# Performance work log

Measured on AMD Instinct MI355X. Metric: run time of the kernel, lower is better.

## Reference

```python
import jax, jax.numpy as jnp
import numpy as np

D_MODEL = 512
NUM_HEADS = 8
HEAD_DIM = D_MODEL // NUM_HEADS  # 64
EMBEDDING_DIM = 512  # undefined global EmbeddingDim in source -> d_model
EVENT_DIM = 388      # undefined global EventDim in source -> MIDI event vocab
B, T = 2, 2048


def setup_inputs() -> dict:
    key = jax.random.key(0)
    ks = jax.random.split(key, 12)
    sc = 0.02
    v = jax.random.normal(ks[0], (B, T, D_MODEL), jnp.float32)
    k = jax.random.normal(ks[1], (B, T, D_MODEL), jnp.float32)
    q = jax.random.normal(ks[2], (B, T, D_MODEL), jnp.float32)
    mask = jnp.tril(jnp.ones((T, T), jnp.float32))  # causal mask, broadcasts to [H,B,T,T]
    Wq = jax.random.normal(ks[3], (D_MODEL, HEAD_DIM), jnp.float32) * sc
    bq = jnp.zeros((HEAD_DIM,), jnp.float32)
    Wk = jax.random.normal(ks[4], (D_MODEL, HEAD_DIM), jnp.float32) * sc
    bk = jnp.zeros((HEAD_DIM,), jnp.float32)
    Wv = jax.random.normal(ks[5], (D_MODEL, HEAD_DIM), jnp.float32) * sc
    bv = jnp.zeros((HEAD_DIM,), jnp.float32)
    E = jax.random.normal(ks[6], (NUM_HEADS, T, HEAD_DIM), jnp.float32) * sc
    Wo = jax.random.normal(ks[7], (D_MODEL, EMBEDDING_DIM), jnp.float32) * sc
    bo = jnp.zeros((EMBEDDING_DIM,), jnp.float32)
    Wl = jax.random.normal(ks[8], (EMBEDDING_DIM, EVENT_DIM), jnp.float32) * sc
    bl = jnp.zeros((EVENT_DIM,), jnp.float32)
    return {"v": v, "k": k, "q": q, "mask": mask, "Wq": Wq, "bq": bq,
            "Wk": Wk, "bk": bk, "Wv": Wv, "bv": bv, "E": E,
            "Wo": Wo, "bo": bo, "Wl": Wl, "bl": bl}


def _skew(S):
    # S: [H,B,T,T] -> Music-Transformer skew via left-pad, reshape, slice
    H, Bb, Tt, _ = S.shape
    S = jnp.pad(S, ((0, 0), (0, 0), (0, 0), (1, 0)))          # [H,B,T,T+1]
    S = S.reshape(H, Bb, Tt + 1, Tt)                           # [H,B,T+1,T]
    return S[:, :, 1:]                                         # [H,B,T,T]


def reference(v, k, q, mask, Wq, bq, Wk, bk, Wv, bv, E, Wo, bo, Wl, bl):
    # The source applies the SAME Dense per head, so all heads share q/k/v projections
    qh = q @ Wq + bq  # [B,T,hd]
    kh = k @ Wk + bk  # [B,T,hd]
    vh = v @ Wv + bv  # [B,T,hd]
    # relative-position scores per head: Q @ E^T then skew
    S = jnp.einsum('btd,hsd->hbts', qh, E)  # [H,B,T,T]
    S = _skew(S)
    qk = jnp.einsum('btd,bsd->bts', qh, kh)  # [B,T,T], identical across heads
    attn = (qk[None] + S) / np.sqrt(HEAD_DIM)  # [H,B,T,T]
    attn = attn * mask - jnp.asarray(1e10, attn.dtype) * (1.0 - mask)
    score = jax.nn.softmax(attn, axis=-1)
    ctx = jnp.einsum('hbts,bsd->hbtd', score, vh)  # [H,B,T,hd]
    ctx = jnp.transpose(ctx, (1, 2, 0, 3)).reshape(ctx.shape[1], ctx.shape[2], -1)  # [B,T,d_model]
    ctx = jax.nn.relu(ctx @ Wo + bo)  # [B,T,EmbeddingDim]
    logits = ctx @ Wl + bl            # [B,T,EventDim]
    return logits
```

## Files before the change

kernel.cpp:

```cpp
#include <hip/hip_runtime.h>
#include <hip/hip_bf16.h>


#define B_ 2
#define T_ 2048
#define DM_ 512
#define H_ 8
#define HD_ 64
#define ED_ 512
#define EV_ 388
#define BT_ (B_ * T_)

typedef __attribute__((ext_vector_type(8))) short short8;
typedef __attribute__((ext_vector_type(4))) float floatx4;

#define MFMA(a, b, c) __builtin_amdgcn_mfma_f32_16x16x32_bf16((a), (b), (c), 0, 0, 0)

__device__ __forceinline__ float bfs(unsigned short s) {
  union { unsigned int i; float f; } v; v.i = ((unsigned int)s) << 16; return v.f;
}
__device__ __forceinline__ unsigned short f2bf(float f) {
  __hip_bfloat16 h = __float2bfloat16(f);
  union { __hip_bfloat16 h; unsigned short u; } v; v.h = h; return v.u;
}
__device__ __forceinline__ float ldf(const void* p, int i, bool isbf) {
  return isbf ? bfs(((const unsigned short*)p)[i]) : ((const float*)p)[i];
}
__device__ __forceinline__ bool det_bf(const unsigned int* mask) {
  return mask[0] != 0x3F800000u;
}
__device__ __forceinline__ void gl_lds16(const unsigned short* g, void* l) {
  __builtin_amdgcn_global_load_lds(
      (const __attribute__((address_space(1))) void*)g,
      (__attribute__((address_space(3))) void*)l, 16, 0, 0);
}

__global__ __launch_bounds__(256) void prep_kernel(
    const void* __restrict__ E, const void* __restrict__ Wq,
    const void* __restrict__ Wk, const void* __restrict__ Wv,
    const void* __restrict__ Wo, const void* __restrict__ Wl,
    const unsigned int* __restrict__ mask,
    unsigned short* __restrict__ E_c, unsigned short* __restrict__ WqT,
    unsigned short* __restrict__ WkT, unsigned short* __restrict__ WvT,
    unsigned short* __restrict__ WoT, unsigned short* __restrict__ WlT) {
  const bool isbf = det_bf(mask);
  const int tid = threadIdx.x;
  int bi = blockIdx.x;
  if (bi < 1024) {
    const int i0 = (bi * 256 + tid) * 4;
    if (isbf) {
      *(uint2*)&E_c[i0] = *(const uint2*)((const unsigned short*)E + i0);
    } else {
      float4 f = *(const float4*)((const float*)E + i0);
      unsigned short p[4] = {f2bf(f.x), f2bf(f.y), f2bf(f.z), f2bf(f.w)};
      *(uint2*)&E_c[i0] = *(uint2*)p;
    }
    return;
  }
  bi -= 1024;
  const void* src; unsigned short* dst; int N, nb;
  if (bi < 16)       { src = Wq; dst = WqT; N = 64;  nb = bi; }
  else if (bi < 32)  { src = Wk; dst = WkT; N = 64;  nb = bi - 16; }
  else if (bi < 48)  { src = Wv; dst = WvT; N = 64;  nb = bi - 32; }
  else if (bi < 176) { src = Wo; dst = WoT; N = 512; nb = bi - 48; }
  else               { src = Wl; dst = WlT; N = 388; nb = bi - 176; }
  const int n = nb * 4 + (tid >> 6);
  const int k0 = (tid & 63) * 8;
  unsigned short vv[8];
#pragma unroll
  for (int j = 0; j < 8; ++j) {
    if (n >= N) vv[j] = 0;
    else if (isbf) vv[j] = ((const unsigned short*)src)[(size_t)(k0 + j) * N + n];
    else vv[j] = f2bf(((const float*)src)[(size_t)(k0 + j) * N + n]);
  }
  *(uint4*)&dst[(size_t)n * DM_ + k0] = *(uint4*)vv;
}

__global__ __launch_bounds__(256) void gemm_proj(
    const void* __restrict__ xq, const void* __restrict__ xk,
    const void* __restrict__ xv,
    const unsigned short* __restrict__ WqT, const unsigned short* __restrict__ WkT,
    const unsigned short* __restrict__ WvT,
    const void* __restrict__ bq, const void* __restrict__ bk,
    const void* __restrict__ bv, const unsigned int* __restrict__ mask,
    unsigned short* __restrict__ oq, unsigned short* __restrict__ ok,
    unsigned short* __restrict__ ovt) {
  __shared__ __align__(16) short sA[64][72];
  __shared__ __align__(16) short sW[64][72];
  const int sel = blockIdx.y;
  const void* x = (sel == 0) ? xq : (sel == 1) ? xk : xv;
  const unsigned short* WT = (sel == 0) ? WqT : (sel == 1) ? WkT : WvT;
  const void* bias = (sel == 0) ? bq : (sel == 1) ? bk : bv;
  const bool isbf = det_bf(mask);

  const int tid = threadIdx.x;
  const int w = tid >> 6, lane = tid & 63;
  const int q_ = lane >> 4, n_ = lane & 15;
  const int row0 = blockIdx.x * 64;

  floatx4 acc[4];
#pragma unroll
  for (int j = 0; j < 4; ++j) acc[j] = (floatx4){0.f, 0.f, 0.f, 0.f};

  for (int k0 = 0; k0 < DM_; k0 += 64) {
    if (isbf) {
#pragma unroll
      for (int it = 0; it < 2; ++it) {
        int idx = tid + it * 256;
        int rr = idx >> 3, cc = (idx & 7) * 8;
        *(uint4*)&sA[rr][cc] =
            *(const uint4*)((const unsigned short*)x + (size_t)(row0 + rr) * DM_ + k0 + cc);
      }
    } else {
#pragma unroll
      for (int it = 0; it < 4; ++it) {
        int idx = tid + it * 256;
        int rr = idx >> 4, cc = (idx & 15) * 4;
        float4 f = *(const float4*)((const float*)x + (size_t)(row0 + rr) * DM_ + k0 + cc);
        unsigned short p[4] = {f2bf(f.x), f2bf(f.y), f2bf(f.z), f2bf(f.w)};
        *(uint2*)&sA[rr][cc] = *(uint2*)p;
      }
    }
#pragma unroll
    for (int it = 0; it < 2; ++it) {
      int idx = tid + it * 256;
      int rr = idx >> 3, cc = (idx & 7) * 8;
      *(uint4*)&sW[rr][cc] = *(const uint4*)(WT + (size_t)rr * DM_ + k0 + cc);
    }
    __syncthreads();
    short8 a0 = *(const short8*)&sA[16 * w + n_][8 * q_];
    short8 a1 = *(const short8*)&sA[16 * w + n_][32 + 8 * q_];
#pragma unroll
    for (int nb = 0; nb < 4; ++nb) {
      short8 b0 = *(const short8*)&sW[16 * nb + n_][8 * q_];
      short8 b1 = *(const short8*)&sW[16 * nb + n_][32 + 8 * q_];
      acc[nb] = MFMA(a0, b0, acc[nb]);
      acc[nb] = MFMA(a1, b1, acc[nb]);
    }
    __syncthreads();
  }

#pragma unroll
  for (int nb = 0; nb < 4; ++nb) {
    const int col = 16 * nb + n_;
    const float bb = ldf(bias, col, isbf);
#pragma unroll
    for (int r = 0; r < 4; ++r) {
      int row = row0 + 16 * w + 4 * q_ + r;
      unsigned short val = f2bf(acc[nb][r] + bb);
      if (sel < 2) {
        unsigned short* o = (sel == 0) ? oq : ok;
        o[(size_t)row * HD_ + col] = val;
      } else {
        int b = row >> 11, s = row & 2047;
        ovt[(((size_t)(b * HD_ + col)) << 11) + s] = val;
      }
    }
  }
}

__device__ __forceinline__ int pbase_of(int ti) {
  return (ti < 16) ? (ti - 8) * 2 : (ti < 24) ? 16 + (ti - 16) * 3
                                              : 40 + (ti - 24) * 4;
}

__global__ __launch_bounds__(256, 2) void attn_kernel(
    const unsigned short* __restrict__ qh, const unsigned short* __restrict__ kh,
    const unsigned short* __restrict__ vt, const unsigned short* __restrict__ E,
    unsigned short* __restrict__ ctxo, float* __restrict__ pc,
    float* __restrict__ ml) {
  __shared__ __align__(16) short sK[2][64][64];
  __shared__ __align__(16) short sVT[3][64][64];
  __shared__ __align__(16) short sE[2][128][64];
  __shared__ __align__(16) short sP[64][64];

  const int id = blockIdx.x;
  const int hb = id & 15;
  const int rem = 79 - (id >> 4);
  int ti, c, nc;
  if (rem < 8)       { ti = rem;                 c = 0;            nc = 1; }
  else if (rem < 24) { ti = 8 + ((rem - 8) >> 1);  c = (rem - 8) & 1;  nc = 2; }
  else if (rem < 48) { ti = 16 + (rem - 24) / 3;   c = (rem - 24) % 3; nc = 3; }
  else               { ti = 24 + ((rem - 48) >> 2); c = (rem - 48) & 3; nc = 4; }
  const int nsteps = ti + 1;
  const int klo = (c * nsteps) / nc;
  const int khi = ((c + 1) * nsteps) / nc;

  const int h = hb >> 1, b = hb & 1;
  const int t0 = ti * 64;

  const int tid = threadIdx.x;
  const int w = tid >> 6, lane = tid & 63;
  const int q_ = lane >> 4, n_ = lane & 15;

  const int trow = t0 + 16 * w + n_;
  const unsigned short* qp = qh + (((size_t)((b << 11) + trow)) << 6) + (q_ << 3);
  const short8 qa0 = *(const short8*)qp;
  const short8 qa1 = *(const short8*)(qp + 32);

  short8 onesf;
#pragma unroll
  for (int j = 0; j < 8; ++j) onesf[j] = (short)0x3F80;

  floatx4 ctxa[4];
#pragma unroll
  for (int nb = 0; nb < 4; ++nb) ctxa[nb] = (floatx4){0.f, 0.f, 0.f, 0.f};
  floatx4 lacc = (floatx4){0.f, 0.f, 0.f, 0.f};

  const unsigned short* eb = E + ((size_t)h << 17);
  const unsigned short* kbase = kh + (((size_t)(b << 11)) << 6);
  const unsigned short* vbase = vt + (((size_t)(b << 6)) << 11);

  const int lrow8 = lane >> 3;
  const int lch = ((lane & 7) ^ lrow8) << 3;
  const int rK0 = 8 * w + lrow8;
  const int c0s = ((q_ ^ (n_ & 7)) << 3);
  const int c1s = (((q_ | 4) ^ (n_ & 7)) << 3);

#define STAGE(kbuf, vbuf, s0v)                                                 \
  {                                                                            \
    const unsigned short* gK =                                                 \
        kbase + (((size_t)((s0v) + rK0)) << 6) + lch;                          \
    const unsigned short* gV =                                                 \
        vbase + (((size_t)rK0) << 11) + (s0v) + lch;                           \
    gl_lds16(gK, (void*)&sK[kbuf][8 * w][0]);                                  \
    gl_lds16(gK + (32 << 6), (void*)(&sK[kbuf][8 * w][0] + 32 * 64));          \
    gl_lds16(gV, (void*)&sVT[vbuf][8 * w][0]);                                 \
    gl_lds16(gV + (32 << 11), (void*)(&sVT[vbuf][8 * w][0] + 32 * 64));        \
    const int rbE = (T_ - 64) + (s0v)-t0;                                      \
    _Pragma("unroll") for (int off = 0; off < 4; ++off) {                      \
      int gr = rbE + 32 * w + 8 * off + lrow8;                                 \
      if (gr > T_ - 1) gr = T_ - 1;           \
      gl_lds16(eb + ((size_t)gr << 6) + lch,                                   \
               (void*)&sE[kbuf][32 * w + 8 * off][0]);                         \
    }                                                                          \
  }

  STAGE(0, 0, klo * 64);

  short8 pa0p = {0, 0, 0, 0, 0, 0, 0, 0};
  short8 pa1p = {0, 0, 0, 0, 0, 0, 0, 0};

  for (int kt = klo; kt < khi; ++kt) {
    const int ph = (kt - klo) & 1;
    const int vcur = (kt - klo) % 3;
    const int s0 = kt * 64;

    asm volatile("s_waitcnt vmcnt(0)" ::: "memory");
    __builtin_amdgcn_sched_barrier(0);
    __builtin_amdgcn_s_barrier();
    __builtin_amdgcn_sched_barrier(0);

    if (kt + 1 < khi) STAGE(ph ^ 1, (kt + 1 - klo) % 3, s0 + 64);

    floatx4 qk[4];
    __builtin_amdgcn_s_setprio(1);
#pragma unroll
    for (int nb = 0; nb < 4; ++nb) {
      short8 kb0 = *(const short8*)&sK[ph][16 * nb + n_][c0s];
      short8 kb1 = *(const short8*)&sK[ph][16 * nb + n_][c1s];
      qk[nb] = (floatx4){0.f, 0.f, 0.f, 0.f};
      qk[nb] = MFMA(qa0, kb0, qk[nb]);
      qk[nb] = MFMA(qa1, kb1, qk[nb]);
    }
    floatx4 qe[5];
#pragma unroll
    for (int f = 0; f < 5; ++f) {
      const short* ep = &sE[ph][16 * (3 - w + f) + n_][0];
      short8 eb0 = *(const short8*)(ep + c0s);
      short8 eb1 = *(const short8*)(ep + c1s);
      qe[f] = (floatx4){0.f, 0.f, 0.f, 0.f};
      qe[f] = MFMA(qa0, eb0, qe[f]);
      qe[f] = MFMA(qa1, eb1, qe[f]);
    }
    if (kt > klo) {
      const int vprev = (vcur + 2) % 3;
#pragma unroll
      for (int nb = 0; nb < 4; ++nb) {
        short8 v0 = *(const short8*)&sVT[vprev][16 * nb + n_][c0s];
        short8 v1 = *(const short8*)&sVT[vprev][16 * nb + n_][c1s];
        ctxa[nb] = MFMA(pa0p, v0, ctxa[nb]);
        ctxa[nb] = MFMA(pa1p, v1, ctxa[nb]);
      }
      lacc = MFMA(pa0p, onesf, lacc);
      lacc = MFMA(pa1p, onesf, lacc);
    }
    __builtin_amdgcn_s_setprio(0);

    const bool diag = (kt == ti);
#pragma unroll
    for (int r = 0; r < 4; ++r) {
      const int t = 4 * q_ + r;
      const int ba = ((q_ << 4) | ((n_ - t + 15) & 15)) << 2;
      const int nd = (n_ + t + 1) & 15;
      const bool hi = nd > t;
      const int swr = (t & 7) << 3;
#pragma unroll
      for (int mb = 0; mb < 4; ++mb) {
        float merged = hi ? qe[mb + 1][r] : qe[mb][r];
        float g = __int_as_float(
            __builtin_amdgcn_ds_bpermute(ba, __float_as_int(merged)));
        float sv = qk[mb][r] + g;
        if (diag && (16 * mb + n_ > 16 * w + t)) sv = -1.0e30f;
        sP[16 * w + t][(16 * mb + n_) ^ swr] =
            (short)f2bf(exp2f(sv * 0.18033688011f));
      }
    }

    pa0p = *(const short8*)&sP[16 * w + n_][c0s];
    pa1p = *(const short8*)&sP[16 * w + n_][c1s];
  }
#undef STAGE

  {
    const int vlast = (khi - 1 - klo) % 3;
    __builtin_amdgcn_s_setprio(1);
#pragma unroll
    for (int nb = 0; nb < 4; ++nb) {
      short8 v0 = *(const short8*)&sVT[vlast][16 * nb + n_][c0s];
      short8 v1 = *(const short8*)&sVT[vlast][16 * nb + n_][c1s];
      ctxa[nb] = MFMA(pa0p, v0, ctxa[nb]);
      ctxa[nb] = MFMA(pa1p, v1, ctxa[nb]);
    }
    lacc = MFMA(pa0p, onesf, lacc);
    lacc = MFMA(pa1p, onesf, lacc);
    __builtin_amdgcn_s_setprio(0);
  }

  if (nc == 1) {
#pragma unroll
    for (int r = 0; r < 4; ++r) {
      const float inv = 1.0f / lacc[r];
      const int row = t0 + 16 * w + 4 * q_ + r;
      const size_t base = (((size_t)((b << 11) + row)) << 9) + (h << 6) + n_;
#pragma unroll
      for (int nb = 0; nb < 4; ++nb)
        ctxo[base + 16 * nb] = f2bf(ctxa[nb][r] * inv);
    }
  } else {
    const int idx = hb * 72 + pbase_of(ti) + c;
    float* pcb = pc + ((size_t)idx << 12);
    float* mlb = ml + ((size_t)idx << 6);
#pragma unroll
    for (int r = 0; r < 4; ++r) {
      const int row = 16 * w + 4 * q_ + r;
#pragma unroll
      for (int nb = 0; nb < 4; ++nb)
        pcb[(row << 6) + 16 * nb + n_] = ctxa[nb][r];
      if (n_ == 0) mlb[row] = lacc[r];
    }
  }
}

__global__ __launch_bounds__(256) void combine_kernel(
    const float* __restrict__ pc, const float* __restrict__ ml,
    unsigned short* __restrict__ ctxo) {
  const int cb = blockIdx.x;
  const int hb = cb / 24;
  const int ti = 8 + cb % 24;
  const int nc = (ti >> 3) + 1;
  const int h = hb >> 1, b = hb & 1, t0 = ti * 64;
  const int tid = threadIdx.x;
  const int row = tid >> 2, seg = (tid & 3) * 16;
  const int idx0 = hb * 72 + pbase_of(ti);

  float lsum = 0.f;
  float4 a4[4];
#pragma unroll
  for (int j = 0; j < 4; ++j) a4[j] = (float4){0.f, 0.f, 0.f, 0.f};
  for (int c = 0; c < nc; ++c) {
    const int idx = idx0 + c;
    lsum += ml[((size_t)idx << 6) + row];
    const float* cp = pc + ((size_t)idx << 12) + (row << 6) + seg;
#pragma unroll
    for (int j = 0; j < 4; ++j) {
      float4 x = *(const float4*)(cp + 4 * j);
      a4[j].x += x.x; a4[j].y += x.y; a4[j].z += x.z; a4[j].w += x.w;
    }
  }
  const float inv = 1.0f / lsum;
  unsigned short o[16];
#pragma unroll
  for (int j = 0; j < 4; ++j) {
    o[4 * j + 0] = f2bf(a4[j].x * inv);
    o[4 * j + 1] = f2bf(a4[j].y * inv);
    o[4 * j + 2] = f2bf(a4[j].z * inv);
    o[4 * j + 3] = f2bf(a4[j].w * inv);
  }
  unsigned short* dst =
      ctxo + (((size_t)((b << 11) + t0 + row)) << 9) + (h << 6) + seg;
  *(uint4*)dst = *(uint4*)&o[0];
  *(uint4*)(dst + 8) = *(uint4*)&o[8];
}

template <int RELU>
__global__ __launch_bounds__(256) void mlp_mfma(
    const unsigned short* __restrict__ A, const unsigned short* __restrict__ WT,
    const void* __restrict__ bias, unsigned short* __restrict__ outBF,
    void* __restrict__ outD, const unsigned int* __restrict__ mask) {
  __shared__ __align__(16) short sA[64][72];
  __shared__ __align__(16) short sW[64][72];
  const int tid = threadIdx.x;
  const int w = tid >> 6, lane = tid & 63;
  const int q_ = lane >> 4, n_ = lane & 15;
  const int row0 = blockIdx.x * 64;
  const int n0 = blockIdx.y * 64;
  const bool isbf = det_bf(mask);

  floatx4 acc[4];
#pragma unroll
  for (int j = 0; j < 4; ++j) acc[j] = (floatx4){0.f, 0.f, 0.f, 0.f};

  for (int k0 = 0; k0 < DM_; k0 += 64) {
#pragma unroll
    for (int it = 0; it < 2; ++it) {
      int idx = tid + it * 256;
      int rr = idx >> 3, cc = (idx & 7) * 8;
      *(uint4*)&sA[rr][cc] = *(const uint4*)(A + (size_t)(row0 + rr) * DM_ + k0 + cc);
      *(uint4*)&sW[rr][cc] = *(const uint4*)(WT + (size_t)(n0 + rr) * DM_ + k0 + cc);
    }
    __syncthreads();
    short8 a0 = *(const short8*)&sA[16 * w + n_][8 * q_];
    short8 a1 = *(const short8*)&sA[16 * w + n_][32 + 8 * q_];
#pragma unroll
    for (int nb = 0; nb < 4; ++nb) {
      short8 b0 = *(const short8*)&sW[16 * nb + n_][8 * q_];
      short8 b1 = *(const short8*)&sW[16 * nb + n_][32 + 8 * q_];
      acc[nb] = MFMA(a0, b0, acc[nb]);
      acc[nb] = MFMA(a1, b1, acc[nb]);
    }
    __syncthreads();
  }

#pragma unroll
  for (int nb = 0; nb < 4; ++nb) {
    const int col = n0 + 16 * nb + n_;
    float bb = 0.f;
    if (RELU || col < EV_) bb = ldf(bias, col, isbf);
#pragma unroll
    for (int r = 0; r < 4; ++r) {
      const int row = row0 + 16 * w + 4 * q_ + r;
      float v = acc[nb][r] + bb;
      if (RELU) {
        outBF[(size_t)row * ED_ + col] = f2bf(fmaxf(v, 0.f));
      } else if (col < EV_) {
        if (isbf) ((unsigned short*)outD)[(size_t)row * EV_ + col] = f2bf(v);
        else      ((float*)outD)[(size_t)row * EV_ + col] = v;
      }
    }
  }
}

extern "C" void kernel_launch(void* const* d_in, const int* in_sizes, int n_in,
                              void* d_out, int out_size, void* d_ws, size_t ws_size,
                              hipStream_t stream) {
  const void* v  = d_in[0];
  const void* k  = d_in[1];
  const void* q  = d_in[2];
  const unsigned int* mask = (const unsigned int*)d_in[3];
  const void* Wq = d_in[4];
  const void* bq = d_in[5];
  const void* Wk = d_in[6];
  const void* bk = d_in[7];
  const void* Wv = d_in[8];
  const void* bv = d_in[9];
  const void* E  = d_in[10];
  const void* Wo = d_in[11];
  const void* bo = d_in[12];
  const void* Wl = d_in[13];
  const void* bl = d_in[14];

  char* p = (char*)d_ws;
  unsigned short* E_c  = (unsigned short*)p; p += (size_t)H_ * T_ * HD_ * 2;
  unsigned short* qhb  = (unsigned short*)p; p += (size_t)BT_ * HD_ * 2;
  unsigned short* khb  = (unsigned short*)p; p += (size_t)BT_ * HD_ * 2;
  unsigned short* vtb  = (unsigned short*)p; p += (size_t)BT_ * HD_ * 2;
  unsigned short* WqT  = (unsigned short*)p; p += (size_t)HD_ * DM_ * 2;
  unsigned short* WkT  = (unsigned short*)p; p += (size_t)HD_ * DM_ * 2;
  unsigned short* WvT  = (unsigned short*)p; p += (size_t)HD_ * DM_ * 2;
  unsigned short* WoT  = (unsigned short*)p; p += (size_t)ED_ * DM_ * 2;
  unsigned short* WlT  = (unsigned short*)p; p += (size_t)448 * DM_ * 2;
  unsigned short* ctxb = (unsigned short*)p; p += (size_t)BT_ * DM_ * 2;
  unsigned short* h1b  = (unsigned short*)p; p += (size_t)BT_ * ED_ * 2;
  float* pc = (float*)p; p += (size_t)16 * 72 * 4096 * 4;
  float* ml = (float*)p; p += (size_t)16 * 72 * 64 * 4;

  prep_kernel<<<dim3(1312), 256, 0, stream>>>(
      E, Wq, Wk, Wv, Wo, Wl, mask, E_c, WqT, WkT, WvT, WoT, WlT);
  gemm_proj<<<dim3(BT_ / 64, 3), 256, 0, stream>>>(
      q, k, v, WqT, WkT, WvT, bq, bk, bv, mask, qhb, khb, vtb);
  attn_kernel<<<dim3(1280), 256, 0, stream>>>(qhb, khb, vtb, E_c, ctxb, pc, ml);
  combine_kernel<<<dim3(384), 256, 0, stream>>>(pc, ml, ctxb);
  mlp_mfma<1><<<dim3(BT_ / 64, ED_ / 64), 256, 0, stream>>>(
      ctxb, WoT, bo, h1b, nullptr, mask);
  mlp_mfma<0><<<dim3(BT_ / 64, 448 / 64), 256, 0, stream>>>(
      h1b, WlT, bl, nullptr, d_out, mask);
}
```

Measured before the change: 206.7 us.

## Reuse overlapping E panels via 3-slot ring and split waitcnts for finer pipelining

Result: no change. 203.8 us (-1.4%).

```diff
diff --git a/kernel.cpp b/kernel.cpp
--- a/kernel.cpp
+++ b/kernel.cpp
@@ -171,7 +171,7 @@
     float* __restrict__ ml) {
   __shared__ __align__(16) short sK[2][64][64];
   __shared__ __align__(16) short sVT[3][64][64];
-  __shared__ __align__(16) short sE[2][128][64];
+  __shared__ __align__(16) short sE3[3][64][64];
   __shared__ __align__(16) short sP[64][64];
 
   const int id = blockIdx.x;
@@ -217,26 +217,39 @@
   const int c0s = ((q_ ^ (n_ & 7)) << 3);
   const int c1s = (((q_ | 4) ^ (n_ & 7)) << 3);
 
-#define STAGE(kbuf, vbuf, s0v)                                                 \
+#define STAGE_K(kbuf, s0v)                                                     \
   {                                                                            \
     const unsigned short* gK =                                                 \
         kbase + (((size_t)((s0v) + rK0)) << 6) + lch;                          \
+    gl_lds16(gK, (void*)&sK[kbuf][8 * w][0]);                                  \
+    gl_lds16(gK + (32 << 6), (void*)(&sK[kbuf][8 * w][0] + 32 * 64));          \
+  }
+#define STAGE_E(slot, panel)                                                   \
+  {                                                                            \
+    _Pragma("unroll") for (int j = 0; j < 2; ++j) {                            \
+      int gr = 64 * (panel) + 16 * w + 8 * j + lrow8;                          \
+      if (gr > T_ - 1) gr = T_ - 1;           \
+      gl_lds16(eb + ((size_t)gr << 6) + lch,                                   \
+               (void*)&sE3[slot][16 * w + 8 * j][0]);                          \
+    }                                                                          \
+  }
+#define STAGE_V(vbuf, s0v)                                                     \
+  {                                                                            \
     const unsigned short* gV =                                                 \
         vbase + (((size_t)rK0) << 11) + (s0v) + lch;                           \
-    gl_lds16(gK, (void*)&sK[kbuf][8 * w][0]);                                  \
-    gl_lds16(gK + (32 << 6), (void*)(&sK[kbuf][8 * w][0] + 32 * 64));          \
     gl_lds16(gV, (void*)&sVT[vbuf][8 * w][0]);                                 \
     gl_lds16(gV + (32 << 11), (void*)(&sVT[vbuf][8 * w][0] + 32 * 64));        \
-    const int rbE = (T_ - 64) + (s0v)-t0;                                      \
-    _Pragma("unroll") for (int off = 0; off < 4; ++off) {                      \
-      int gr = rbE + 32 * w + 8 * off + lrow8;                                 \
-      if (gr > T_ - 1) gr = T_ - 1;           \
-      gl_lds16(eb + ((size_t)gr << 6) + lch,                                   \
-               (void*)&sE[kbuf][32 * w + 8 * off][0]);                         \
-    }                                                                          \
-  }
-
-  STAGE(0, 0, klo * 64);
+  }
+
+  {
+    const int p0 = 31 + klo - ti;
+    STAGE_K(0, klo * 64);
+    __builtin_amdgcn_sched_barrier(0);
+    STAGE_E(p0 % 3, p0);
+    STAGE_E((p0 + 1) % 3, p0 + 1);
+    __builtin_amdgcn_sched_barrier(0);
+    STAGE_V(0, klo * 64);
+  }
 
   short8 pa0p = {0, 0, 0, 0, 0, 0, 0, 0};
   short8 pa1p = {0, 0, 0, 0, 0, 0, 0, 0};
@@ -245,13 +258,22 @@
     const int ph = (kt - klo) & 1;
     const int vcur = (kt - klo) % 3;
     const int s0 = kt * 64;
-
-    asm volatile("s_waitcnt vmcnt(0)" ::: "memory");
+    const int pk = 31 + kt - ti;
+    const int slotA = pk % 3;
+    const int slotB = (pk + 1) % 3;
+
+    asm volatile("s_waitcnt vmcnt(4)" ::: "memory");
     __builtin_amdgcn_sched_barrier(0);
     __builtin_amdgcn_s_barrier();
     __builtin_amdgcn_sched_barrier(0);
 
-    if (kt + 1 < khi) STAGE(ph ^ 1, (kt + 1 - klo) % 3, s0 + 64);
+    if (kt + 1 < khi) {
+      STAGE_K(ph ^ 1, s0 + 64);
+      __builtin_amdgcn_sched_barrier(0);
+      STAGE_E((pk + 2) % 3, pk + 2);
+      __builtin_amdgcn_sched_barrier(0);
+      STAGE_V((kt + 1 - klo) % 3, s0 + 64);
+    }
 
     floatx4 qk[4];
     __builtin_amdgcn_s_setprio(1);
@@ -262,16 +284,6 @@
       qk[nb] = (floatx4){0.f, 0.f, 0.f, 0.f};
       qk[nb] = MFMA(qa0, kb0, qk[nb]);
       qk[nb] = MFMA(qa1, kb1, qk[nb]);
-    }
-    floatx4 qe[5];
-#pragma unroll
-    for (int f = 0; f < 5; ++f) {
-      const short* ep = &sE[ph][16 * (3 - w + f) + n_][0];
-      short8 eb0 = *(const short8*)(ep + c0s);
-      short8 eb1 = *(const short8*)(ep + c1s);
-      qe[f] = (floatx4){0.f, 0.f, 0.f, 0.f};
-      qe[f] = MFMA(qa0, eb0, qe[f]);
-      qe[f] = MFMA(qa1, eb1, qe[f]);
     }
     if (kt > klo) {
       const int vprev = (vcur + 2) % 3;
@@ -286,6 +298,30 @@
       lacc = MFMA(pa1p, onesf, lacc);
     }
     __builtin_amdgcn_s_setprio(0);
+
+    if (kt + 1 < khi) {
+      asm volatile("s_waitcnt vmcnt(8)" ::: "memory");
+    } else {
+      asm volatile("s_waitcnt vmcnt(2)" ::: "memory");
+    }
+    __builtin_amdgcn_sched_barrier(0);
+    __builtin_amdgcn_s_barrier();
+    __builtin_amdgcn_sched_barrier(0);
+
+    floatx4 qe[5];
+#pragma unroll
+    for (int f = 0; f < 5; ++f) {
+      const int row16 = 16 * (3 - w + f);
+      const short* ep = (row16 < 64) ? &sE3[slotA][row16 + n_][0]
+                                     : &sE3[slotB][row16 - 64 + n_][0];
+      short8 eb0 = *(const short8*)(ep + c0s);
+      short8 eb1 = *(const short8*)(ep + c1s);
+      qe[f] = (floatx4){0.f, 0.f, 0.f, 0.f};
+      __builtin_amdgcn_s_setprio(1);
+      qe[f] = MFMA(qa0, eb0, qe[f]);
+      qe[f] = MFMA(qa1, eb1, qe[f]);
+      __builtin_amdgcn_s_setprio(0);
+    }
 
     const bool diag = (kt == ti);
 #pragma unroll
@@ -310,8 +346,14 @@
     pa0p = *(const short8*)&sP[16 * w + n_][c0s];
     pa1p = *(const short8*)&sP[16 * w + n_][c1s];
   }
-#undef STAGE
-
+#undef STAGE_K
+#undef STAGE_E
+#undef STAGE_V
+
+  asm volatile("s_waitcnt vmcnt(0)" ::: "memory");
+  __builtin_amdgcn_sched_barrier(0);
+  __builtin_amdgcn_s_barrier();
+  __builtin_amdgcn_sched_barrier(0);
   {
     const int vlast = (khi - 1 - klo) % 3;
     __builtin_amdgcn_s_setprio(1);
```
